# Optimization experiments

Hardware: AMD Instinct MI355X
Metric: run time of the kernel (lower is better)

Reference implementation:

```python
import jax, jax.numpy as jnp
import numpy as np

MAX_S, MIN_S, MAX_R = 3.0, 0.5, 3.0
A = (MAX_S - MIN_S) / 2.0   # 1.25
B = (MAX_S + MIN_S) / 2.0   # 1.75
C = (MAX_R - 1.0) / 2.0     # 1.0
D = (MAX_R + 1.0) / 2.0     # 2.0

# 3x3 kernel base points, row-major: dim0 = dy, dim1 = dx, shape [2, 9]
BASE = jnp.array([[-1, -1], [-1, 0], [-1, 1], [0, -1], [0, 0], [0, 1],
                  [1, -1], [1, 0], [1, 1]], dtype=jnp.float32).T


def conv2d(x, w, b=None):
    y = jax.lax.conv_general_dilated(x, w, window_strides=(1, 1),
                                     padding=((1, 1), (1, 1)),
                                     dimension_numbers=('NCHW', 'OIHW', 'NCHW'))
    if b is not None:
        y = y + b[None, :, None, None]
    return y


def setup_inputs() -> dict:
    key = jax.random.key(0)
    ks = jax.random.split(key, 8)
    return {
        'x': jax.random.normal(ks[0], (8, 64, 128, 128), jnp.float32),
        'w_main': jax.random.normal(ks[1], (64, 64, 3, 3), jnp.float32) * 0.05,
        'w_rot': jax.random.normal(ks[2], (2, 64, 3, 3), jnp.float32) * 0.05,
        'b_rot': jax.random.normal(ks[3], (2,), jnp.float32) * 0.05,
        'w_str': jax.random.normal(ks[4], (1, 64, 3, 3), jnp.float32) * 0.05,
        'b_str': jax.random.normal(ks[5], (1,), jnp.float32) * 0.05,
        'w_whl': jax.random.normal(ks[6], (1, 64, 3, 3), jnp.float32) * 0.05,
        'b_whl': jax.random.normal(ks[7], (1,), jnp.float32) * 0.05,
    }


def reference(x, w_main, w_rot, b_rot, w_str, b_str, w_whl, b_whl):
    b, c, H, W = x.shape
    K = 9
    # --- offset generation ---
    rot = conv2d(x, w_rot, b_rot)                     # [b,2,H,W]
    sin, cos = rot[:, 0], rot[:, 1]
    norm = jnp.sqrt(sin ** 2 + cos ** 2 + 1e-6)
    sin, cos = sin / norm, cos / norm
    r = jnp.tanh(conv2d(x, w_str, b_str))[:, 0] * A + B   # [b,H,W]
    wr = jnp.tanh(conv2d(x, w_whl, b_whl))[:, 0] * C + D  # [b,H,W]
    ky, kx = BASE[0], BASE[1]                             # [9]
    kyb = ky[None, :, None, None]
    kxb = kx[None, :, None, None]
    o0 = kyb * (wr * r)[:, None]                          # [b,9,H,W]
    o1 = kxb * wr[:, None]
    sinb, cosb = sin[:, None], cos[:, None]
    dy = cosb * o0 + sinb * o1 - kyb                      # rotation then subtract base
    dx = -sinb * o0 + cosb * o1 - kxb
    # --- deformable sampling positions (stride=1, pad=1, dil=1) ---
    py = jnp.arange(H, dtype=x.dtype)[None, None, :, None] + kyb + dy  # [b,9,H,W]
    px = jnp.arange(W, dtype=x.dtype)[None, None, None, :] + kxb + dx
    y0f = jnp.floor(py); x0f = jnp.floor(px)
    ly = py - y0f; lx = px - x0f
    y0 = y0f.astype(jnp.int32); x0 = x0f.astype(jnp.int32)
    x_flat = x.reshape(b, c, H * W)

    def gather(yi, xi, wgt):
        valid = (yi >= 0) & (yi < H) & (xi >= 0) & (xi < W)
        idx = jnp.clip(yi, 0, H - 1) * W + jnp.clip(xi, 0, W - 1)
        g = jnp.take_along_axis(x_flat, idx.reshape(b, 1, -1), axis=2)
        g = g.reshape(b, c, K, H, W)
        return g * (wgt * valid)[:, None]

    val = (gather(y0, x0, (1 - ly) * (1 - lx))
           + gather(y0, x0 + 1, (1 - ly) * lx)
           + gather(y0 + 1, x0, ly * (1 - lx))
           + gather(y0 + 1, x0 + 1, ly * lx))          # [b,c,9,H,W]
    # final 3x3 conv over sampled points == contraction over (c, k)
    out = jnp.einsum('bckhw,ock->bohw', val, w_main.reshape(w_main.shape[0], c, K))
    return out
```

## Files before the change

kernel.cpp:

```cpp
#include <hip/hip_runtime.h>
#include <hip/hip_bf16.h>
#include <hip/hip_fp16.h>
#include <math.h>

#define HH 128
#define WW 128
#define HWSZ (HH*WW)
#define CH 64
#define OC 64
#define NB 8

#define TH 16
#define TW 8
#define RGR 36
#define RGC 28
#define RPX2 (RGR*RGC)
#define NQ (RPX2*4)
#define NCHUNK (NQ/64)

#define XT_BYTES   (16777216u)
#define OFFS_BYTES (2097152u)

typedef _Float16 f16x8 __attribute__((ext_vector_type(8)));
typedef __attribute__((ext_vector_type(4))) float f32x4_t;

__global__ __launch_bounds__(256) void transpose_kernel(
    const float* __restrict__ x, const float* __restrict__ w_main,
    __half* __restrict__ xT, __half* __restrict__ wmT2)
{
    const int t = threadIdx.x;
    const int i = blockIdx.x;
    if (i >= 2048) {
        const int base = (i - 2048) * 4096 + t * 16;
        #pragma unroll
        for (int j = 0; j < 16; ++j) {
            const int e = base + j;
            const int k = e >> 12;
            const int r = e & 4095;
            const int o = r >> 6;
            const int c = r & 63;
            wmT2[e] = __float2half(w_main[(size_t)o * (CH * 9) + c * 9 + k]);
        }
        return;
    }
    __shared__ float tile[64][65];
    const int b = i & 7;
    const int j = i >> 3;
    const int h  = j >> 1;
    const int w0 = (j & 1) * 64;
    const float* xb = x + (size_t)b * CH * HWSZ + h * WW + w0;
    {
        const int w = t & 63, c0 = (t >> 6) * 16;
        #pragma unroll
        for (int jj = 0; jj < 16; ++jj)
            tile[c0 + jj][w] = xb[(size_t)(c0 + jj) * HWSZ + w];
    }
    __syncthreads();
    {
        const int c = t & 63, wq = t >> 6;
        __half* o = xT + ((size_t)b * HWSZ + h * WW + w0) * 64;
        #pragma unroll
        for (int jj = 0; jj < 16; ++jj) {
            const int w = wq * 16 + jj;
            o[(size_t)w * 64 + c] = __float2half(tile[c][w]);
        }
    }
}

__global__ __launch_bounds__(256) void offsets_kernel(
    const float* __restrict__ x,
    const float* __restrict__ w_rot,
    const float* __restrict__ w_str,
    const float* __restrict__ w_whl,
    float4* __restrict__ part)
{
    __shared__ float xs[8][4][WW];
    const int t  = threadIdx.x;
    const int i  = blockIdx.x;
    const int b  = i & 7;
    const int rp = (i >> 3) & 63;
    const int cg = i >> 9;
    const int h0 = rp * 2;
    const int c0 = cg * 8;
    const float* xb = x + (size_t)b * CH * HWSZ;
    #pragma unroll
    for (int jj = 0; jj < 4; ++jj) {
        const int u   = t + jj * 256;
        const int ch  = u >> 7;
        const int rem = u & 127;
        const int row = rem >> 5;
        const int w4  = (rem & 31) * 4;
        const int grow = h0 - 1 + row;
        float4 v = make_float4(0.f, 0.f, 0.f, 0.f);
        if (grow >= 0 && grow < HH)
            v = *(const float4*)&xb[((size_t)(c0 + ch) * HH + grow) * WW + w4];
        *(float4*)&xs[ch][row][w4] = v;
    }
    __syncthreads();
    const int r = t >> 7, w = t & 127;
    const int wl = max(w - 1, 0), wr2 = min(w + 1, WW - 1);
    const float ml = (w > 0) ? 1.f : 0.f, mr = (w < WW - 1) ? 1.f : 0.f;
    float a0 = 0.f, a1 = 0.f, a2 = 0.f, a3 = 0.f;
    #pragma unroll
    for (int ch = 0; ch < 8; ++ch) {
        const int cc = c0 + ch;
        #pragma unroll
        for (int dy = 0; dy < 3; ++dy) {
            const float* row_ = &xs[ch][r + dy][0];
            const float nl = row_[wl] * ml;
            const float nc = row_[w];
            const float nr = row_[wr2] * mr;
            const int d0 = cc * 9 + dy * 3;
            a0 = fmaf(nl, w_rot[d0 + 0], a0); a0 = fmaf(nc, w_rot[d0 + 1], a0); a0 = fmaf(nr, w_rot[d0 + 2], a0);
            a1 = fmaf(nl, w_rot[576 + d0 + 0], a1); a1 = fmaf(nc, w_rot[576 + d0 + 1], a1); a1 = fmaf(nr, w_rot[576 + d0 + 2], a1);
            a2 = fmaf(nl, w_str[d0 + 0], a2); a2 = fmaf(nc, w_str[d0 + 1], a2); a2 = fmaf(nr, w_str[d0 + 2], a2);
            a3 = fmaf(nl, w_whl[d0 + 0], a3); a3 = fmaf(nc, w_whl[d0 + 1], a3); a3 = fmaf(nr, w_whl[d0 + 2], a3);
        }
    }
    part[((size_t)cg * NB + b) * HWSZ + (h0 + r) * WW + w] = make_float4(a0, a1, a2, a3);
}

__global__ __launch_bounds__(256) void reduce_kernel(
    const float4* __restrict__ part,
    const float* __restrict__ b_rot, const float* __restrict__ b_str,
    const float* __restrict__ b_whl, float4* __restrict__ offs)
{
    const int i = blockIdx.x * 256 + threadIdx.x;
    float4 s = make_float4(0.f, 0.f, 0.f, 0.f);
    #pragma unroll
    for (int cg = 0; cg < 8; ++cg) {
        const float4 p = part[(size_t)cg * NB * HWSZ + i];
        s.x += p.x; s.y += p.y; s.z += p.z; s.w += p.w;
    }
    float sv = s.x + b_rot[0], cv = s.y + b_rot[1];
    const float inv = 1.0f / sqrtf(sv * sv + cv * cv + 1e-6f);
    const float rr = tanhf(s.z + b_str[0]) * 1.25f + 1.75f;
    const float wq = tanhf(s.w + b_whl[0]) * 1.0f + 2.0f;
    offs[i] = make_float4(sv * inv, cv * inv, wq * rr, wq);
}

__global__ __launch_bounds__(512, 4) void deform_kernel(
    const __half* __restrict__ xT, const __half* __restrict__ wmT2,
    const float4* __restrict__ offs, float* __restrict__ out)
{
    __shared__ union {
        uint4 xs[NQ];
        float ots[128][67];
    } sh;
    const int t  = threadIdx.x;
    const int wv = t >> 6;
    const int l  = t & 63;
    const int lm = l & 15;
    const int lg = l >> 4;
    const int i  = blockIdx.x;
    const int b  = i & 7;
    const int tile = i >> 3;
    const int w0 = (tile & 15) * TW;
    const int h0 = (tile >> 4) * TH;
    const int pi = wv * 16 + lm;
    const int h = h0 + (pi >> 3);
    const int w = w0 + (pi & 7);
    const __half* xb = xT + (size_t)b * HWSZ * 64;

    const float4 o4 = offs[(size_t)b * HWSZ + h * WW + w];

    auto stage = [&](int g) {
        for (int c = wv; c < NCHUNK; c += 8) {
            const int u   = c * 64 + l;
            const int pxu = u >> 2;
            const int sq  = u & 3;
            const int lr  = pxu / RGC;
            const int lc  = pxu - lr * RGC;
            const int gy  = min(max(h0 - 10 + lr, 0), HH - 1);
            const int gx  = min(max(w0 - 10 + lc, 0), WW - 1);
            const int sq2 = sq ^ (pxu & 3);
            const __half* gp = xb + ((size_t)(gy * WW + gx) * 64 + g * 32 + sq2 * 8);
            __builtin_amdgcn_global_load_lds(
                (const __attribute__((address_space(1))) void*)gp,
                (__attribute__((address_space(3))) void*)((char*)sh.xs + (size_t)c * 1024),
                16, 0, 0);
        }
    };

    stage(0);

    const float sv = o4.x, cv = o4.y, av = o4.z, wvl = o4.w;
    const float hh  = (float)h;
    const float wwf = (float)w;

    int ti[9], td[9];
    __half2 w2[9][4];
    #pragma unroll
    for (int k = 0; k < 9; ++k) {
        const float kyf = (float)(k / 3) - 1.f;
        const float kxf = (float)(k % 3) - 1.f;
        const float o0v = kyf * av;
        const float o1v = kxf * wvl;
        const float pyf = hh  + cv * o0v + sv * o1v;
        const float pxf = wwf - sv * o0v + cv * o1v;
        const float y0f = floorf(pyf), x0f = floorf(pxf);
        const float ly = pyf - y0f, lx = pxf - x0f;
        const int y0 = (int)y0f, x0i = (int)x0f;
        const int y1 = y0 + 1, x1 = x0i + 1;
        const bool vy0 = (y0 >= 0) && (y0 < HH);
        const bool vy1 = (y1 >= 0) && (y1 < HH);
        const bool vx0 = (x0i >= 0) && (x0i < WW);
        const bool vx1 = (x1 >= 0) && (x1 < WW);
        w2[k][0] = __float2half2_rn((1.f - ly) * (1.f - lx) * ((vy0 && vx0) ? 1.f : 0.f));
        w2[k][1] = __float2half2_rn((1.f - ly) * lx         * ((vy0 && vx1) ? 1.f : 0.f));
        w2[k][2] = __float2half2_rn(ly * (1.f - lx)         * ((vy1 && vx0) ? 1.f : 0.f));
        w2[k][3] = __float2half2_rn(ly * lx                 * ((vy1 && vx1) ? 1.f : 0.f));
        const int iy0 = min(max(y0, 0), HH - 1), iy1 = min(max(y1, 0), HH - 1);
        const int ix0 = min(max(x0i, 0), WW - 1), ix1 = min(max(x1, 0), WW - 1);
        ti[k] = (iy0 - (h0 - 10)) * RGC + (ix0 - (w0 - 10));
        td[k] = (ix1 - ix0) | ((iy1 - iy0) << 1);
    }

    f32x4_t acc0 = {0.f, 0.f, 0.f, 0.f};
    f32x4_t acc1 = acc0, acc2 = acc0, acc3 = acc0;

    auto compute = [&](int g) {
        const int cb0 = g * 32 + lg * 8;
        #pragma unroll
        for (int k = 0; k < 9; ++k) {
            const int i00 = ti[k];
            const int dxx = td[k] & 1;
            const int dyy = (td[k] >> 1) * RGC;
            const int i01 = i00 + dxx;
            const int i10 = i00 + dyy;
            const int i11 = i10 + dxx;
            union Q { uint4 q; __half2 h2[4]; };
            Q q00, q01, q10, q11;
            q00.q = sh.xs[i00 * 4 + (lg ^ (i00 & 3))];
            q01.q = sh.xs[i01 * 4 + (lg ^ (i01 & 3))];
            q10.q = sh.xs[i10 * 4 + (lg ^ (i10 & 3))];
            q11.q = sh.xs[i11 * 4 + (lg ^ (i11 & 3))];
            union { __half2 h2[4]; f16x8 v; } af;
            #pragma unroll
            for (int j = 0; j < 4; ++j) {
                af.h2[j] = __hfma2(q00.h2[j], w2[k][0],
                           __hfma2(q01.h2[j], w2[k][1],
                           __hfma2(q10.h2[j], w2[k][2],
                           __hmul2(q11.h2[j], w2[k][3]))));
            }
            const __half* wp = wmT2 + ((size_t)k * 64 + lm) * 64 + cb0;
            const f16x8 bf0 = *(const f16x8*)(wp);
            const f16x8 bf1 = *(const f16x8*)(wp + 1024);
            const f16x8 bf2v = *(const f16x8*)(wp + 2048);
            const f16x8 bf3 = *(const f16x8*)(wp + 3072);
            acc0 = __builtin_amdgcn_mfma_f32_16x16x32_f16(af.v, bf0,  acc0, 0, 0, 0);
            acc1 = __builtin_amdgcn_mfma_f32_16x16x32_f16(af.v, bf1,  acc1, 0, 0, 0);
            acc2 = __builtin_amdgcn_mfma_f32_16x16x32_f16(af.v, bf2v, acc2, 0, 0, 0);
            acc3 = __builtin_amdgcn_mfma_f32_16x16x32_f16(af.v, bf3,  acc3, 0, 0, 0);
        }
    };

    __syncthreads();
    compute(0);
    __syncthreads();
    stage(1);
    __syncthreads();
    compute(1);

    __syncthreads();
    const int pxw = wv * 16 + lg * 4;
    #pragma unroll
    for (int rg2 = 0; rg2 < 4; ++rg2) {
        sh.ots[pxw + rg2][ 0 + lm] = acc0[rg2];
        sh.ots[pxw + rg2][16 + lm] = acc1[rg2];
        sh.ots[pxw + rg2][32 + lm] = acc2[rg2];
        sh.ots[pxw + rg2][48 + lm] = acc3[rg2];
    }
    __syncthreads();
    const int oo = t >> 3;
    const int s  = t & 7;
    #pragma unroll
    for (int j2 = 0; j2 < 4; ++j2) {
        const int idx  = s * 4 + j2;
        const int r    = idx >> 1;
        const int colh = idx & 1;
        const int p0   = r * 8 + colh * 4;
        float4 v = make_float4(sh.ots[p0 + 0][oo], sh.ots[p0 + 1][oo],
                               sh.ots[p0 + 2][oo], sh.ots[p0 + 3][oo]);
        *(float4*)&out[((size_t)b * OC + oo) * HWSZ +
                       (h0 + r) * WW + w0 + colh * 4] = v;
    }
}

extern "C" void kernel_launch(void* const* d_in, const int* in_sizes, int n_in,
                              void* d_out, int out_size, void* d_ws, size_t ws_size,
                              hipStream_t stream)
{
    const float* x      = (const float*)d_in[0];
    const float* w_main = (const float*)d_in[1];
    const float* w_rot  = (const float*)d_in[2];
    const float* b_rot  = (const float*)d_in[3];
    const float* w_str  = (const float*)d_in[4];
    const float* b_str  = (const float*)d_in[5];
    const float* w_whl  = (const float*)d_in[6];
    const float* b_whl  = (const float*)d_in[7];
    float* out = (float*)d_out;

    char* ws = (char*)d_ws;
    __half*  xT   = (__half*)ws;
    float4*  offs = (float4*)(ws + XT_BYTES);
    __half*  wmT2 = (__half*)(ws + XT_BYTES + OFFS_BYTES);
    float4*  part = (float4*)d_out;

    transpose_kernel<<<dim3(2057), 256, 0, stream>>>(x, w_main, xT, wmT2);
    offsets_kernel<<<dim3(4096), 256, 0, stream>>>(x, w_rot, w_str, w_whl, part);
    reduce_kernel<<<dim3(NB * HWSZ / 256), 256, 0, stream>>>(
        part, b_rot, b_str, b_whl, offs);
    deform_kernel<<<dim3(1024), 512, 0, stream>>>(xT, wmT2, offs, out);
}
```

Before: 225.1 us.

## Merge transpose and offsets kernels; register-prefetch second channel half in deform

Merges the transpose and offset-partial kernels into a single launch that dispatches on block index, which removes one launch and lets the two phases run side by side. In the deform kernel, the async global_load_lds staging is replaced by plain vector loads into LDS. The second 32-channel half is now prefetched into registers before the first compute pass and written to LDS afterwards, so its global latency overlaps the first compute. The LDS swizzle changes to use (pxu>>1)&3. The register prefetch adds eight uint4 per thread, which raises register pressure under launch bounds (512, 4).

```diff
diff --git a/kernel.cpp b/kernel.cpp
--- a/kernel.cpp
+++ b/kernel.cpp
@@ -14,9 +14,8 @@
 #define TW 8
 #define RGR 36
 #define RGC 28
-#define RPX2 (RGR*RGC)
-#define NQ (RPX2*4)
-#define NCHUNK (NQ/64)
+#define RPXB (RGR*RGC)
+#define NQB (RPXB*4)
 
 #define XT_BYTES   (16777216u)
 #define OFFS_BYTES (2097152u)
@@ -24,14 +23,19 @@
 typedef _Float16 f16x8 __attribute__((ext_vector_type(8)));
 typedef __attribute__((ext_vector_type(4))) float f32x4_t;
 
-__global__ __launch_bounds__(256) void transpose_kernel(
+__global__ __launch_bounds__(256) void pre_kernel(
     const float* __restrict__ x, const float* __restrict__ w_main,
-    __half* __restrict__ xT, __half* __restrict__ wmT2)
+    const float* __restrict__ w_rot, const float* __restrict__ w_str,
+    const float* __restrict__ w_whl,
+    __half* __restrict__ xT, __half* __restrict__ wmT2,
+    float4* __restrict__ part)
 {
+    __shared__ float shmem[64 * 65];
     const int t = threadIdx.x;
     const int i = blockIdx.x;
-    if (i >= 2048) {
-        const int base = (i - 2048) * 4096 + t * 16;
+
+    if (i >= 6144) {
+        const int base = (i - 6144) * 4096 + t * 16;
         #pragma unroll
         for (int j = 0; j < 16; ++j) {
             const int e = base + j;
@@ -43,40 +47,35 @@
         }
         return;
     }
-    __shared__ float tile[64][65];
-    const int b = i & 7;
-    const int j = i >> 3;
-    const int h  = j >> 1;
-    const int w0 = (j & 1) * 64;
-    const float* xb = x + (size_t)b * CH * HWSZ + h * WW + w0;
-    {
-        const int w = t & 63, c0 = (t >> 6) * 16;
-        #pragma unroll
-        for (int jj = 0; jj < 16; ++jj)
-            tile[c0 + jj][w] = xb[(size_t)(c0 + jj) * HWSZ + w];
-    }
-    __syncthreads();
-    {
-        const int c = t & 63, wq = t >> 6;
-        __half* o = xT + ((size_t)b * HWSZ + h * WW + w0) * 64;
-        #pragma unroll
-        for (int jj = 0; jj < 16; ++jj) {
-            const int w = wq * 16 + jj;
-            o[(size_t)w * 64 + c] = __float2half(tile[c][w]);
-        }
-    }
-}
-
-__global__ __launch_bounds__(256) void offsets_kernel(
-    const float* __restrict__ x,
-    const float* __restrict__ w_rot,
-    const float* __restrict__ w_str,
-    const float* __restrict__ w_whl,
-    float4* __restrict__ part)
-{
-    __shared__ float xs[8][4][WW];
-    const int t  = threadIdx.x;
-    const int i  = blockIdx.x;
+
+    if (i >= 4096) {
+        float (*tile)[65] = (float(*)[65])shmem;
+        const int it = i - 4096;
+        const int b = it & 7;
+        const int j = it >> 3;
+        const int h  = j >> 1;
+        const int w0 = (j & 1) * 64;
+        const float* xb = x + (size_t)b * CH * HWSZ + h * WW + w0;
+        {
+            const int w = t & 63, c0 = (t >> 6) * 16;
+            #pragma unroll
+            for (int jj = 0; jj < 16; ++jj)
+                tile[c0 + jj][w] = xb[(size_t)(c0 + jj) * HWSZ + w];
+        }
+        __syncthreads();
+        {
+            const int c = t & 63, wq = t >> 6;
+            __half* o = xT + ((size_t)b * HWSZ + h * WW + w0) * 64;
+            #pragma unroll
+            for (int jj = 0; jj < 16; ++jj) {
+                const int w = wq * 16 + jj;
+                o[(size_t)w * 64 + c] = __float2half(tile[c][w]);
+            }
+        }
+        return;
+    }
+
+    float (*xs)[4][WW] = (float(*)[4][WW])shmem;
     const int b  = i & 7;
     const int rp = (i >> 3) & 63;
     const int cg = i >> 9;
@@ -144,7 +143,7 @@
     const float4* __restrict__ offs, float* __restrict__ out)
 {
     __shared__ union {
-        uint4 xs[NQ];
+        uint4 xs[NQB];
         float ots[128][67];
     } sh;
     const int t  = threadIdx.x;
@@ -163,27 +162,6 @@
     const __half* xb = xT + (size_t)b * HWSZ * 64;
 
     const float4 o4 = offs[(size_t)b * HWSZ + h * WW + w];
-
-    auto stage = [&](int g) {
-        for (int c = wv; c < NCHUNK; c += 8) {
-            const int u   = c * 64 + l;
-            const int pxu = u >> 2;
-            const int sq  = u & 3;
-            const int lr  = pxu / RGC;
-            const int lc  = pxu - lr * RGC;
-            const int gy  = min(max(h0 - 10 + lr, 0), HH - 1);
-            const int gx  = min(max(w0 - 10 + lc, 0), WW - 1);
-            const int sq2 = sq ^ (pxu & 3);
-            const __half* gp = xb + ((size_t)(gy * WW + gx) * 64 + g * 32 + sq2 * 8);
-            __builtin_amdgcn_global_load_lds(
-                (const __attribute__((address_space(1))) void*)gp,
-                (__attribute__((address_space(3))) void*)((char*)sh.xs + (size_t)c * 1024),
-                16, 0, 0);
-        }
-    };
-
-    stage(0);
-
     const float sv = o4.x, cv = o4.y, av = o4.z, wvl = o4.w;
     const float hh  = (float)h;
     const float wwf = (float)w;
@@ -221,6 +199,7 @@
 
     auto compute = [&](int g) {
         const int cb0 = g * 32 + lg * 8;
+        const __half* wb = wmT2 + lm * 64 + cb0;
         #pragma unroll
         for (int k = 0; k < 9; ++k) {
             const int i00 = ti[k];
@@ -231,10 +210,10 @@
             const int i11 = i10 + dxx;
             union Q { uint4 q; __half2 h2[4]; };
             Q q00, q01, q10, q11;
-            q00.q = sh.xs[i00 * 4 + (lg ^ (i00 & 3))];
-            q01.q = sh.xs[i01 * 4 + (lg ^ (i01 & 3))];
-            q10.q = sh.xs[i10 * 4 + (lg ^ (i10 & 3))];
-            q11.q = sh.xs[i11 * 4 + (lg ^ (i11 & 3))];
+            q00.q = sh.xs[i00 * 4 + (lg ^ ((i00 >> 1) & 3))];
+            q01.q = sh.xs[i01 * 4 + (lg ^ ((i01 >> 1) & 3))];
+            q10.q = sh.xs[i10 * 4 + (lg ^ ((i10 >> 1) & 3))];
+            q11.q = sh.xs[i11 * 4 + (lg ^ ((i11 >> 1) & 3))];
             union { __half2 h2[4]; f16x8 v; } af;
             #pragma unroll
             for (int j = 0; j < 4; ++j) {
@@ -243,7 +222,7 @@
                            __hfma2(q10.h2[j], w2[k][2],
                            __hmul2(q11.h2[j], w2[k][3]))));
             }
-            const __half* wp = wmT2 + ((size_t)k * 64 + lm) * 64 + cb0;
+            const __half* wp = wb + (size_t)k * 4096;
             const f16x8 bf0 = *(const f16x8*)(wp);
             const f16x8 bf1 = *(const f16x8*)(wp + 1024);
             const f16x8 bf2v = *(const f16x8*)(wp + 2048);
@@ -255,10 +234,43 @@
         }
     };
 
+    #pragma unroll
+    for (int j = 0; j < 8; ++j) {
+        const int u = t + j * 512;
+        if (u < NQB) {
+            const int pxu = u >> 2, q = u & 3;
+            const int lr = pxu / RGC;
+            const int lc = pxu - lr * RGC;
+            const int gy = min(max(h0 - 10 + lr, 0), HH - 1);
+            const int gx = min(max(w0 - 10 + lc, 0), WW - 1);
+            sh.xs[pxu * 4 + (q ^ ((pxu >> 1) & 3))] =
+                *(const uint4*)(xb + (size_t)(gy * WW + gx) * 64 + q * 8);
+        }
+    }
+    uint4 s1[8];
+    #pragma unroll
+    for (int j = 0; j < 8; ++j) {
+        const int u = t + j * 512;
+        if (u < NQB) {
+            const int pxu = u >> 2, q = u & 3;
+            const int lr = pxu / RGC;
+            const int lc = pxu - lr * RGC;
+            const int gy = min(max(h0 - 10 + lr, 0), HH - 1);
+            const int gx = min(max(w0 - 10 + lc, 0), WW - 1);
+            s1[j] = *(const uint4*)(xb + (size_t)(gy * WW + gx) * 64 + 32 + q * 8);
+        }
+    }
     __syncthreads();
     compute(0);
     __syncthreads();
-    stage(1);
+    #pragma unroll
+    for (int j = 0; j < 8; ++j) {
+        const int u = t + j * 512;
+        if (u < NQB) {
+            const int pxu = u >> 2, q = u & 3;
+            sh.xs[pxu * 4 + (q ^ ((pxu >> 1) & 3))] = s1[j];
+        }
+    }
     __syncthreads();
     compute(1);
 
@@ -307,8 +319,8 @@
     __half*  wmT2 = (__half*)(ws + XT_BYTES + OFFS_BYTES);
     float4*  part = (float4*)d_out;
 
-    transpose_kernel<<<dim3(2057), 256, 0, stream>>>(x, w_main, xT, wmT2);
-    offsets_kernel<<<dim3(4096), 256, 0, stream>>>(x, w_rot, w_str, w_whl, part);
+    pre_kernel<<<dim3(6153), 256, 0, stream>>>(x, w_main, w_rot, w_str, w_whl,
+                                               xT, wmT2, part);
     reduce_kernel<<<dim3(NB * HWSZ / 256), 256, 0, stream>>>(
         part, b_rot, b_str, b_whl, offs);
     deform_kernel<<<dim3(1024), 512, 0, stream>>>(xT, wmT2, offs, out);
```

Result: slower. 252.8 us (+12.3%).
